# Performance work log

Measured on AMD Instinct MI355X. Metric: run time of the kernel, lower is better.

Reference implementation:

```python
import jax, jax.numpy as jnp
import numpy as np

B = 2048
PARAM_SHAPES = {
    'l1c0': (1, 8, 3, 3), 'l1c1': (3, 4, 8, 2), 'l1c2': (2, 4, 8, 2), 'l1c3': (2, 4, 8, 2), 'l1c4': (2, 4, 8, 1), 'b1': (8, 4, 4, 4, 4),
    'l2c0': (1, 4, 8, 2), 'l2c1': (2, 2, 4, 2), 'l2c2': (2, 2, 4, 2), 'l2c3': (2, 2, 4, 2), 'l2c4': (2, 2, 4, 1), 'b2': (4, 2, 2, 2, 2),
    'l3c0': (1, 2, 4, 2), 'l3c1': (2, 2, 2, 2), 'l3c2': (2, 2, 2, 2), 'l3c3': (2, 2, 2, 2), 'l3c4': (2, 2, 2, 1), 'b3': (2, 2, 2, 2, 2),
    'W': (2, 32), 'bl': (2,),
}

def setup_inputs():
    key = jax.random.key(0)
    ks = jax.random.split(key, len(PARAM_SHAPES) + 1)
    inp = {'x': jax.random.normal(ks[0], (B, 3, 8, 8, 8, 8), dtype=jnp.float32)}
    for k, (name, shp) in zip(ks[1:], PARAM_SHAPES.items()):
        scale = 0.5 if name[0] == 'l' and name != 'bl' else 0.1
        inp[name] = jax.random.normal(k, shp, dtype=jnp.float32) * scale
    return inp

def tt_linear(x, cores, bias):
    # y[b, m1..md] = sum_{n1..nd} W[m1..md, n1..nd] x[b, n1..nd] + bias[m1..md]
    # W is the TT-matrix with cores G_k of shape (r_{k-1}, m_k, n_k, r_k).
    b = x.shape[0]
    z = x.reshape(b, 1, -1)  # (B, rank, flat=[n_k..n_d, m_1..m_{k-1}])
    for G in cores:
        r0, m, n, r1 = G.shape
        z = jnp.einsum('brns,rmnq->bqsm', z.reshape(b, r0, n, -1), G).reshape(b, r1, -1)
    return z.reshape((b,) + bias.shape) + bias

def reference(x, l1c0, l1c1, l1c2, l1c3, l1c4, b1, l2c0, l2c1, l2c2, l2c3, l2c4, b2, l3c0, l3c1, l3c2, l3c3, l3c4, b3, W, bl):
    h = jax.nn.relu(tt_linear(x, [l1c0, l1c1, l1c2, l1c3, l1c4], b1))
    h = jax.nn.relu(tt_linear(h, [l2c0, l2c1, l2c2, l2c3, l2c4], b2))
    h = jax.nn.relu(tt_linear(h, [l3c0, l3c1, l3c2, l3c3, l3c4], b3))
    logits = h.reshape(-1, 32) @ W.T + bl  # (B, 2)
    return jax.nn.log_softmax(logits, axis=1)
```

## Files before the change

### kernel.cpp

```cpp
#include <hip/hip_runtime.h>
#include <math.h>

#define WC3  0
#define WC2  128
#define WU1  256
#define T2S  288
#define T3S  1440
#define H1O  288
#define BO   2528
#define CO   1440
#define DO   1984
#define H2O  2256
#define H3O  2320
#define LDS_FLOATS 3680

__global__ void tt_setup_w3(const float* __restrict__ v0, const float* __restrict__ v1,
                            const float* __restrict__ v2, const float* __restrict__ v3,
                            const float* __restrict__ v4, float* __restrict__ w3) {
    int i = blockIdx.x * 256 + threadIdx.x;
    if (i >= 2048) return;
    int mi = i >> 6, nj = i & 63;
    int m1 = (mi >> 4) & 1, m2 = (mi >> 3) & 1, m3 = (mi >> 2) & 1, m4 = (mi >> 1) & 1, m5 = mi & 1;
    int n1 = (nj >> 4) & 3, n2 = (nj >> 3) & 1, n3 = (nj >> 2) & 1, n4 = (nj >> 1) & 1, n5 = nj & 1;
    float s = 0.f;
#pragma unroll
    for (int q1 = 0; q1 < 2; ++q1) {
        float a1 = v0[(m1 * 4 + n1) * 2 + q1];
#pragma unroll
        for (int q2 = 0; q2 < 2; ++q2) {
            float a2 = a1 * v1[((q1 * 2 + m2) * 2 + n2) * 2 + q2];
#pragma unroll
            for (int q3 = 0; q3 < 2; ++q3) {
                float a3 = a2 * v2[((q2 * 2 + m3) * 2 + n3) * 2 + q3];
#pragma unroll
                for (int q4 = 0; q4 < 2; ++q4)
                    s = fmaf(a3 * v3[((q3 * 2 + m4) * 2 + n4) * 2 + q4],
                             v4[(q4 * 2 + m5) * 2 + n5], s);
            }
        }
    }
    w3[i] = s;
}

#define PREFETCH_X(BUF, SLAB) do {                                          \
    const float4* xq_ = (const float4*)xb + (SLAB) * 512 + t * 8;           \
    _Pragma("unroll")                                                       \
    for (int i_ = 0; i_ < 8; ++i_) {                                        \
        const float4 v_ = xq_[i_];                                          \
        BUF[i_*4+0] = v_.x; BUF[i_*4+1] = v_.y;                             \
        BUF[i_*4+2] = v_.z; BUF[i_*4+3] = v_.w;                             \
    } } while (0)

#define STEP1(BUF) do {                                                     \
    _Pragma("unroll") for (int m5_ = 0; m5_ < 4; ++m5_)                     \
    _Pragma("unroll") for (int q4_ = 0; q4_ < 2; ++q4_) {                   \
        const float* w_ = g4 + (q4_ * 4 + m5_) * 8;                         \
        _Pragma("unroll") for (int n4l_ = 0; n4l_ < 4; ++n4l_) {            \
            float sa_ = BUF[n4l_*8+0] * w_[0];                              \
            _Pragma("unroll") for (int n5_ = 1; n5_ < 8; ++n5_)             \
                sa_ = fmaf(BUF[n4l_*8+n5_], w_[n5_], sa_);                  \
            t1[n4l_*8 + m5_*2 + q4_] = sa_;                                 \
        } } } while (0)

__global__ __launch_bounds__(64)
__attribute__((amdgpu_waves_per_eu(1, 2)))
void tt_main(const float* __restrict__ x,
             const float* __restrict__ g0, const float* __restrict__ g1,
             const float* __restrict__ g2, const float* __restrict__ g3,
             const float* __restrict__ g4, const float* __restrict__ b1g,
             const float* __restrict__ u0, const float* __restrict__ u1,
             const float* __restrict__ u2, const float* __restrict__ u3,
             const float* __restrict__ u4, const float* __restrict__ b2g,
             const float* __restrict__ b3g,
             const float* __restrict__ Wmg, const float* __restrict__ blg,
             const float* __restrict__ w3g,
             float* __restrict__ out)
{
    __shared__ float smem[LDS_FLOATS];
    const int t = threadIdx.x;
    const int b = blockIdx.x;
    const float* xb = x + (size_t)b * 12288;

    float xv0[32], xv1[32], t1[32];

    PREFETCH_X(xv0, 0);
    PREFETCH_X(xv1, 1);

    smem[WC3 + t] = g3[t];  smem[WC3 + 64 + t] = g3[64 + t];
    smem[WC2 + t] = g2[t];  smem[WC2 + 64 + t] = g2[64 + t];
    if (t < 32) smem[WU1 + t] = u1[t];
    __syncthreads();

    const int h = t & 1;
    const int p = t >> 1;

    float regT4[36];
#pragma unroll
    for (int i = 0; i < 36; ++i) regT4[i] = 0.f;

    STEP1(xv0);

#pragma unroll
    for (int s = 0; s < 6; ++s) {
        const int n1 = s >> 1, n2h = s & 1;

        if (s < 4) {
            if (s & 1) { PREFETCH_X(xv1, s + 2); } else { PREFETCH_X(xv0, s + 2); }
        }

        float acc[16];
#pragma unroll
        for (int i = 0; i < 16; ++i) acc[i] = 0.f;
#pragma unroll
        for (int pass = 0; pass < 2; ++pass) {
            const int hh = (pass == 0) ? h : (1 - h);
            if (pass == 1) {
#pragma unroll
                for (int i = 0; i < 32; ++i) t1[i] = __shfl_xor(t1[i], 1);
            }
#pragma unroll
            for (int m4 = 0; m4 < 4; ++m4) {
                const int cbase = WC3 + ((h * 4 + m4) * 8 + hh * 4) * 2;
                const float4 c0 = *(const float4*)&smem[cbase];
                const float4 c1 = *(const float4*)&smem[cbase + 4];
                const float cs[8] = {c0.x, c0.y, c0.z, c0.w, c1.x, c1.y, c1.z, c1.w};
#pragma unroll
                for (int m5 = 0; m5 < 4; ++m5) {
                    float sa = acc[m4*4+m5];
#pragma unroll
                    for (int n4l = 0; n4l < 4; ++n4l)
#pragma unroll
                    for (int q4 = 0; q4 < 2; ++q4)
                        sa = fmaf(t1[n4l*8 + m5*2 + q4], cs[n4l*2 + q4], sa);
                    acc[m4*4+m5] = sa;
                }
            }
        }

        __syncthreads();
#pragma unroll
        for (int m45 = 0; m45 < 16; ++m45)
            smem[T2S + p * 36 + m45 * 2 + h] = acc[m45];
        __syncthreads();

        {
            const int n3h = t & 1;
            const int q2  = (t >> 1) & 1;
            const int m3  = (t >> 2) & 3;
            const int n2l = t >> 4;
            float o3[16];
#pragma unroll
            for (int i = 0; i < 16; ++i) o3[i] = 0.f;
#pragma unroll
            for (int n3l = 0; n3l < 4; ++n3l) {
                const int rb = T2S + (n2l * 8 + n3h * 4 + n3l) * 36;
                float rv[32];
#pragma unroll
                for (int g = 0; g < 8; ++g) {
                    const float4 v = *(const float4*)&smem[rb + g * 4];
                    rv[g*4+0] = v.x; rv[g*4+1] = v.y; rv[g*4+2] = v.z; rv[g*4+3] = v.w;
                }
                const int wb = WC2 + ((q2 * 4 + m3) * 8 + n3h * 4 + n3l) * 2;
                const float w0 = smem[wb], w1 = smem[wb + 1];
#pragma unroll
                for (int m45 = 0; m45 < 16; ++m45)
                    o3[m45] = fmaf(rv[m45*2], w0, fmaf(rv[m45*2+1], w1, o3[m45]));
            }
#pragma unroll
            for (int k = 0; k < 16; ++k) o3[k] += __shfl_xor(o3[k], 1);
            const int row = n2h * 16 + n2l * 4 + m3;
#pragma unroll
            for (int k = 0; k < 8; ++k) {
                const float v = n3h ? o3[8 + k] : o3[k];
                smem[T3S + row * 34 + (n3h * 8 + k) * 2 + q2] = v;
            }
        }

        if (s < 5) {
            if ((s + 1) & 1) { STEP1(xv1); } else { STEP1(xv0); }
        }

        if (n2h == 1) {
            __syncthreads();

            const int m3 = t >> 4, m4 = (t >> 2) & 3, m5 = t & 3;
            float2 zz[8];
#pragma unroll
            for (int n2 = 0; n2 < 8; ++n2)
                zz[n2] = *(const float2*)&smem[T3S + (n2 * 4 + m3) * 34 + (m4 * 4 + m5) * 2];
#pragma unroll
            for (int jj = 0; jj < 4; ++jj)
#pragma unroll
            for (int q1 = 0; q1 < 3; ++q1) {
                float sa = regT4[jj * 9 + n1 * 3 + q1];
#pragma unroll
                for (int n2g = 0; n2g < 4; ++n2g) {
                    const float4 w = *(const float4*)(g1 + ((q1 * 4 + jj) * 8 + n2g * 2) * 2);
                    sa = fmaf(zz[n2g*2].x,   w.x, sa);
                    sa = fmaf(zz[n2g*2].y,   w.y, sa);
                    sa = fmaf(zz[n2g*2+1].x, w.z, sa);
                    sa = fmaf(zz[n2g*2+1].y, w.w, sa);
                }
                regT4[jj * 9 + n1 * 3 + q1] = sa;
            }
        }
    }
    __syncthreads();

#pragma unroll
    for (int jj = 0; jj < 4; ++jj) {
        float bia[8];
#pragma unroll
        for (int m1 = 0; m1 < 8; ++m1) bia[m1] = b1g[m1 * 256 + jj * 64 + t];
#pragma unroll
        for (int m1 = 0; m1 < 8; ++m1) {
            float sa = bia[m1];
#pragma unroll
            for (int n1 = 0; n1 < 3; ++n1)
#pragma unroll
            for (int q1 = 0; q1 < 3; ++q1)
                sa = fmaf(regT4[jj * 9 + n1 * 3 + q1], g0[(m1 * 3 + n1) * 3 + q1], sa);
            smem[H1O + m1 * 256 + jj * 64 + t] = fmaxf(sa, 0.f);
        }
    }
    __syncthreads();

#pragma unroll
    for (int pq = 0; pq < 2; ++pq) {
        const int p3 = 2 * t + pq;
        float o[8];
#pragma unroll
        for (int i = 0; i < 8; ++i) o[i] = 0.f;
#pragma unroll
        for (int n4 = 0; n4 < 4; ++n4) {
            const float4 hv = *(const float4*)&smem[H1O + (p3 * 4 + n4) * 4];
            const float ax = hv.x*u4[0]  + hv.y*u4[1]  + hv.z*u4[2]  + hv.w*u4[3];
            const float ay = hv.x*u4[8]  + hv.y*u4[9]  + hv.z*u4[10] + hv.w*u4[11];
            const float az = hv.x*u4[4]  + hv.y*u4[5]  + hv.z*u4[6]  + hv.w*u4[7];
            const float aw = hv.x*u4[12] + hv.y*u4[13] + hv.z*u4[14] + hv.w*u4[15];
#pragma unroll
            for (int q4 = 0; q4 < 2; ++q4) {
                const float a0 = q4 ? ay : ax;
                const float a1 = q4 ? aw : az;
#pragma unroll
                for (int q3 = 0; q3 < 2; ++q3)
#pragma unroll
                for (int m4 = 0; m4 < 2; ++m4) {
                    const float w = u3[((q3 * 2 + m4) * 4 + n4) * 2 + q4];
                    o[(m4 * 2 + 0) * 2 + q3] = fmaf(a0, w, o[(m4 * 2 + 0) * 2 + q3]);
                    o[(m4 * 2 + 1) * 2 + q3] = fmaf(a1, w, o[(m4 * 2 + 1) * 2 + q3]);
                }
            }
        }
#pragma unroll
        for (int k = 0; k < 8; ++k) smem[BO + p3 * 9 + k] = o[k];
    }
    __syncthreads();

    if (t < 32) {
        float o[16];
#pragma unroll
        for (int i = 0; i < 16; ++i) o[i] = 0.f;
#pragma unroll
        for (int n3 = 0; n3 < 4; ++n3)
#pragma unroll
        for (int q3 = 0; q3 < 2; ++q3) {
            float zb[4];
#pragma unroll
            for (int m45 = 0; m45 < 4; ++m45)
                zb[m45] = smem[BO + (t * 4 + n3) * 9 + m45 * 2 + q3];
#pragma unroll
            for (int m3 = 0; m3 < 2; ++m3)
#pragma unroll
            for (int q2 = 0; q2 < 2; ++q2) {
                const float w = u2[((q2 * 2 + m3) * 4 + n3) * 2 + q3];
#pragma unroll
                for (int m45 = 0; m45 < 4; ++m45)
                    o[(m3 * 4 + m45) * 2 + q2] = fmaf(zb[m45], w, o[(m3 * 4 + m45) * 2 + q2]);
            }
        }
#pragma unroll
        for (int k = 0; k < 16; ++k) smem[CO + t * 17 + k] = o[k];
    }
    __syncthreads();

    if (t < 32) {
        const int n1 = t >> 2, m2 = (t >> 1) & 1, m3 = t & 1;
        float o[8];
#pragma unroll
        for (int i = 0; i < 8; ++i) o[i] = 0.f;
#pragma unroll
        for (int n2 = 0; n2 < 4; ++n2)
#pragma unroll
        for (int q2 = 0; q2 < 2; ++q2) {
            float cb[4];
#pragma unroll
            for (int m45 = 0; m45 < 4; ++m45)
                cb[m45] = smem[CO + (n1 * 4 + n2) * 17 + (m3 * 4 + m45) * 2 + q2];
#pragma unroll
            for (int q1 = 0; q1 < 2; ++q1) {
                const float w = smem[WU1 + ((q1 * 2 + m2) * 4 + n2) * 2 + q2];
#pragma unroll
                for (int m45 = 0; m45 < 4; ++m45)
                    o[m45 * 2 + q1] = fmaf(cb[m45], w, o[m45 * 2 + q1]);
            }
        }
#pragma unroll
        for (int m45 = 0; m45 < 4; ++m45)
#pragma unroll
        for (int q1 = 0; q1 < 2; ++q1)
            smem[DO + (m2 * 8 + m3 * 4 + m45) * 17 + n1 * 2 + q1] = o[m45 * 2 + q1];
    }
    __syncthreads();

    if (t < 16) {
        float o[4];
#pragma unroll
        for (int i = 0; i < 4; ++i) o[i] = 0.f;
#pragma unroll
        for (int n1 = 0; n1 < 8; ++n1)
#pragma unroll
        for (int q1 = 0; q1 < 2; ++q1) {
            const float dv = smem[DO + t * 17 + n1 * 2 + q1];
#pragma unroll
            for (int m1 = 0; m1 < 4; ++m1)
                o[m1] = fmaf(dv, u0[(m1 * 8 + n1) * 2 + q1], o[m1]);
        }
#pragma unroll
        for (int m1 = 0; m1 < 4; ++m1)
            smem[H2O + m1 * 16 + t] = fmaxf(o[m1] + b2g[m1 * 16 + t], 0.f);
    }
    __syncthreads();

    if (t < 32) {
        const float4* wr = (const float4*)(w3g + t * 64);
        float sa = b3g[t];
#pragma unroll
        for (int g = 0; g < 16; ++g) {
            const float4 w4 = wr[g];
            sa = fmaf(w4.x, smem[H2O + g*4 + 0],
                 fmaf(w4.y, smem[H2O + g*4 + 1],
                 fmaf(w4.z, smem[H2O + g*4 + 2],
                 fmaf(w4.w, smem[H2O + g*4 + 3], sa))));
        }
        smem[H3O + t] = fmaxf(sa, 0.f);
    }
    __syncthreads();

    {
        const int k = t & 31;
        float pr = smem[H3O + k] * Wmg[t];
#pragma unroll
        for (int d = 16; d >= 1; d >>= 1) pr += __shfl_xor(pr, d);
        const float l0 = __shfl(pr, 0) + blg[0];
        const float l1 = __shfl(pr, 32) + blg[1];
        if (t == 0) {
            const float mm = fmaxf(l0, l1);
            const float lse = mm + logf(expf(l0 - mm) + expf(l1 - mm));
            out[(size_t)b * 2 + 0] = l0 - lse;
            out[(size_t)b * 2 + 1] = l1 - lse;
        }
    }
}

extern "C" void kernel_launch(void* const* d_in, const int* in_sizes, int n_in,
                              void* d_out, int out_size, void* d_ws, size_t ws_size,
                              hipStream_t stream) {
    const float* x    = (const float*)d_in[0];
    const float* l1c0 = (const float*)d_in[1];
    const float* l1c1 = (const float*)d_in[2];
    const float* l1c2 = (const float*)d_in[3];
    const float* l1c3 = (const float*)d_in[4];
    const float* l1c4 = (const float*)d_in[5];
    const float* b1   = (const float*)d_in[6];
    const float* l2c0 = (const float*)d_in[7];
    const float* l2c1 = (const float*)d_in[8];
    const float* l2c2 = (const float*)d_in[9];
    const float* l2c3 = (const float*)d_in[10];
    const float* l2c4 = (const float*)d_in[11];
    const float* b2   = (const float*)d_in[12];
    const float* l3c0 = (const float*)d_in[13];
    const float* l3c1 = (const float*)d_in[14];
    const float* l3c2 = (const float*)d_in[15];
    const float* l3c3 = (const float*)d_in[16];
    const float* l3c4 = (const float*)d_in[17];
    const float* b3   = (const float*)d_in[18];
    const float* Wm   = (const float*)d_in[19];
    const float* bl   = (const float*)d_in[20];
    float* W3 = (float*)d_ws;

    tt_setup_w3<<<8, 256, 0, stream>>>(l3c0, l3c1, l3c2, l3c3, l3c4, W3);
    tt_main<<<2048, 64, 0, stream>>>(x, l1c0, l1c1, l1c2, l1c3, l1c4, b1,
                                     l2c0, l2c1, l2c2, l2c3, l2c4, b2, b3,
                                     Wm, bl, W3, (float*)d_out);
}
```

Baseline: 218.3 us.

## Process two batch samples per block to interleave independent work and halve grid

```diff
diff --git a/kernel.cpp b/kernel.cpp
--- a/kernel.cpp
+++ b/kernel.cpp
@@ -1,18 +1,26 @@
 #include <hip/hip_runtime.h>
 #include <math.h>
 
-#define WC3  0
-#define WC2  128
-#define WU1  256
-#define T2S  288
-#define T3S  1440
-#define H1O  288
-#define BO   2528
-#define CO   1440
-#define DO   1984
-#define H2O  2256
-#define H3O  2320
-#define LDS_FLOATS 3680
+#define WC3   0
+#define WC2   128
+#define WU1   256
+#define T2A_  288
+#define T3A_  1440
+#define T2B_  2528
+#define T3B_  3680
+#define H1A_  288
+#define H1B_  2528
+#define BO_A  4768
+#define BO_B  5920
+#define CO_A  7072
+#define CO_B  7616
+#define DO_A  8160
+#define DO_B  8432
+#define H2A_  8704
+#define H2B_  8768
+#define H3A_  8832
+#define H3B_  8864
+#define LDS_FLOATS 8896
 
 __global__ void tt_setup_w3(const float* __restrict__ v0, const float* __restrict__ v1,
                             const float* __restrict__ v2, const float* __restrict__ v3,
@@ -42,16 +50,15 @@
     w3[i] = s;
 }
 
-#define PREFETCH_X(BUF, SLAB) do {                                          \
-    const float4* xq_ = (const float4*)xb + (SLAB) * 512 + t * 8;           \
-    _Pragma("unroll")                                                       \
-    for (int i_ = 0; i_ < 8; ++i_) {                                        \
+#define PREFETCH_X(BUF, XB, SLAB) do {                                      \
+    const float4* xq_ = (const float4*)(XB) + (SLAB) * 512 + t * 8;         \
+    _Pragma("unroll") for (int i_ = 0; i_ < 8; ++i_) {                      \
         const float4 v_ = xq_[i_];                                          \
         BUF[i_*4+0] = v_.x; BUF[i_*4+1] = v_.y;                             \
         BUF[i_*4+2] = v_.z; BUF[i_*4+3] = v_.w;                             \
     } } while (0)
 
-#define STEP1(BUF) do {                                                     \
+#define STEP1(T1, BUF) do {                                                 \
     _Pragma("unroll") for (int m5_ = 0; m5_ < 4; ++m5_)                     \
     _Pragma("unroll") for (int q4_ = 0; q4_ < 2; ++q4_) {                   \
         const float* w_ = g4 + (q4_ * 4 + m5_) * 8;                         \
@@ -59,11 +66,97 @@
             float sa_ = BUF[n4l_*8+0] * w_[0];                              \
             _Pragma("unroll") for (int n5_ = 1; n5_ < 8; ++n5_)             \
                 sa_ = fmaf(BUF[n4l_*8+n5_], w_[n5_], sa_);                  \
-            t1[n4l_*8 + m5_*2 + q4_] = sa_;                                 \
+            T1[n4l_*8 + m5_*2 + q4_] = sa_;                                 \
         } } } while (0)
 
+#define STEP2(ACC, T1) do {                                                 \
+    _Pragma("unroll") for (int i_ = 0; i_ < 16; ++i_) ACC[i_] = 0.f;        \
+    _Pragma("unroll") for (int pass_ = 0; pass_ < 2; ++pass_) {             \
+        const int hh_ = (pass_ == 0) ? h : (1 - h);                         \
+        if (pass_ == 1) {                                                   \
+            _Pragma("unroll") for (int i_ = 0; i_ < 32; ++i_)               \
+                T1[i_] = __shfl_xor(T1[i_], 1);                             \
+        }                                                                   \
+        _Pragma("unroll") for (int m4_ = 0; m4_ < 4; ++m4_) {               \
+            const int cb_ = WC3 + ((h * 4 + m4_) * 8 + hh_ * 4) * 2;        \
+            const float4 c0_ = *(const float4*)&smem[cb_];                  \
+            const float4 c1_ = *(const float4*)&smem[cb_ + 4];              \
+            const float cs_[8] = {c0_.x,c0_.y,c0_.z,c0_.w,c1_.x,c1_.y,c1_.z,c1_.w}; \
+            _Pragma("unroll") for (int m5_ = 0; m5_ < 4; ++m5_) {           \
+                float sa_ = ACC[m4_*4+m5_];                                 \
+                _Pragma("unroll") for (int n4l_ = 0; n4l_ < 4; ++n4l_)      \
+                _Pragma("unroll") for (int q4_ = 0; q4_ < 2; ++q4_)         \
+                    sa_ = fmaf(T1[n4l_*8 + m5_*2 + q4_], cs_[n4l_*2+q4_], sa_); \
+                ACC[m4_*4+m5_] = sa_;                                       \
+            } } } } while (0)
+
+#define STEP3(T2X, T3X) do {                                                \
+    const int n3h_ = t & 1, q2_ = (t >> 1) & 1, m3_ = (t >> 2) & 3, n2l_ = t >> 4; \
+    float o3_[16];                                                          \
+    _Pragma("unroll") for (int i_ = 0; i_ < 16; ++i_) o3_[i_] = 0.f;        \
+    _Pragma("unroll") for (int n3l_ = 0; n3l_ < 4; ++n3l_) {                \
+        const int rb_ = (T2X) + (n2l_*8 + n3h_*4 + n3l_) * 36;              \
+        float rv_[32];                                                      \
+        _Pragma("unroll") for (int g_ = 0; g_ < 8; ++g_) {                  \
+            const float4 v_ = *(const float4*)&smem[rb_ + g_*4];            \
+            rv_[g_*4+0]=v_.x; rv_[g_*4+1]=v_.y; rv_[g_*4+2]=v_.z; rv_[g_*4+3]=v_.w; \
+        }                                                                   \
+        const int wb_ = WC2 + ((q2_*4 + m3_)*8 + n3h_*4 + n3l_) * 2;        \
+        const float w0_ = smem[wb_], w1_ = smem[wb_+1];                     \
+        _Pragma("unroll") for (int m45_ = 0; m45_ < 16; ++m45_)             \
+            o3_[m45_] = fmaf(rv_[m45_*2], w0_, fmaf(rv_[m45_*2+1], w1_, o3_[m45_])); \
+    }                                                                       \
+    _Pragma("unroll") for (int k_ = 0; k_ < 16; ++k_) o3_[k_] += __shfl_xor(o3_[k_], 1); \
+    const int row_ = n2h*16 + n2l_*4 + m3_;                                 \
+    _Pragma("unroll") for (int k_ = 0; k_ < 8; ++k_) {                      \
+        const float v_ = n3h_ ? o3_[8+k_] : o3_[k_];                        \
+        smem[(T3X) + row_*34 + (n3h_*8+k_)*2 + q2_] = v_;                   \
+    } } while (0)
+
+#define STEP4(T3X, RT4) do {                                                \
+    const int m3_ = t >> 4, m4_ = (t >> 2) & 3, m5_ = t & 3;                \
+    float2 zz_[8];                                                          \
+    _Pragma("unroll") for (int n2_ = 0; n2_ < 8; ++n2_)                     \
+        zz_[n2_] = *(const float2*)&smem[(T3X) + (n2_*4+m3_)*34 + (m4_*4+m5_)*2]; \
+    _Pragma("unroll") for (int jj_ = 0; jj_ < 4; ++jj_)                     \
+    _Pragma("unroll") for (int q1_ = 0; q1_ < 3; ++q1_) {                   \
+        float sa_ = RT4[jj_*9 + n1*3 + q1_];                                \
+        _Pragma("unroll") for (int n2g_ = 0; n2g_ < 4; ++n2g_) {            \
+            const float4 w_ = *(const float4*)(g1 + ((q1_*4+jj_)*8 + n2g_*2)*2); \
+            sa_ = fmaf(zz_[n2g_*2].x,   w_.x, sa_);                         \
+            sa_ = fmaf(zz_[n2g_*2].y,   w_.y, sa_);                         \
+            sa_ = fmaf(zz_[n2g_*2+1].x, w_.z, sa_);                         \
+            sa_ = fmaf(zz_[n2g_*2+1].y, w_.w, sa_);                         \
+        }                                                                   \
+        RT4[jj_*9 + n1*3 + q1_] = sa_;                                      \
+    } } while (0)
+
+#define L2AB(H1X, BOX) do {                                                 \
+    _Pragma("unroll") for (int pq_ = 0; pq_ < 2; ++pq_) {                   \
+        const int p3_ = 2*t + pq_;                                          \
+        float o_[8];                                                        \
+        _Pragma("unroll") for (int i_ = 0; i_ < 8; ++i_) o_[i_] = 0.f;      \
+        _Pragma("unroll") for (int n4_ = 0; n4_ < 4; ++n4_) {               \
+            const float4 hv_ = *(const float4*)&smem[(H1X) + (p3_*4+n4_)*4]; \
+            const float ax_ = hv_.x*u4[0]  + hv_.y*u4[1]  + hv_.z*u4[2]  + hv_.w*u4[3];  \
+            const float ay_ = hv_.x*u4[8]  + hv_.y*u4[9]  + hv_.z*u4[10] + hv_.w*u4[11]; \
+            const float az_ = hv_.x*u4[4]  + hv_.y*u4[5]  + hv_.z*u4[6]  + hv_.w*u4[7];  \
+            const float aw_ = hv_.x*u4[12] + hv_.y*u4[13] + hv_.z*u4[14] + hv_.w*u4[15]; \
+            _Pragma("unroll") for (int q4_ = 0; q4_ < 2; ++q4_) {           \
+                const float a0_ = q4_ ? ay_ : ax_;                          \
+                const float a1_ = q4_ ? aw_ : az_;                          \
+                _Pragma("unroll") for (int q3_ = 0; q3_ < 2; ++q3_)         \
+                _Pragma("unroll") for (int m4_ = 0; m4_ < 2; ++m4_) {       \
+                    const float w_ = u3[((q3_*2+m4_)*4+n4_)*2+q4_];         \
+                    o_[(m4_*2+0)*2+q3_] = fmaf(a0_, w_, o_[(m4_*2+0)*2+q3_]); \
+                    o_[(m4_*2+1)*2+q3_] = fmaf(a1_, w_, o_[(m4_*2+1)*2+q3_]); \
+                } } }                                                       \
+        _Pragma("unroll") for (int k_ = 0; k_ < 8; ++k_)                    \
+            smem[(BOX) + p3_*9 + k_] = o_[k_];                              \
+    } } while (0)
+
 __global__ __launch_bounds__(64)
-__attribute__((amdgpu_waves_per_eu(1, 2)))
+__attribute__((amdgpu_waves_per_eu(1, 1)))
 void tt_main(const float* __restrict__ x,
              const float* __restrict__ g0, const float* __restrict__ g1,
              const float* __restrict__ g2, const float* __restrict__ g3,
@@ -79,12 +172,12 @@
     __shared__ float smem[LDS_FLOATS];
     const int t = threadIdx.x;
     const int b = blockIdx.x;
-    const float* xb = x + (size_t)b * 12288;
-
-    float xv0[32], xv1[32], t1[32];
-
-    PREFETCH_X(xv0, 0);
-    PREFETCH_X(xv1, 1);
+    const float* xbA = x + (size_t)(2 * b) * 12288;
+    const float* xbB = xbA + 12288;
+
+    float xvA[32], xvB[32];
+    PREFETCH_X(xvA, xbA, 0);
+    PREFETCH_X(xvB, xbB, 0);
 
     smem[WC3 + t] = g3[t];  smem[WC3 + 64 + t] = g3[64 + t];
     smem[WC2 + t] = g2[t];  smem[WC2 + 64 + t] = g2[64 + t];
@@ -94,116 +187,42 @@
     const int h = t & 1;
     const int p = t >> 1;
 
-    float regT4[36];
-#pragma unroll
-    for (int i = 0; i < 36; ++i) regT4[i] = 0.f;
-
-    STEP1(xv0);
-
-#pragma unroll
-    for (int s = 0; s < 6; ++s) {
-        const int n1 = s >> 1, n2h = s & 1;
-
-        if (s < 4) {
-            if (s & 1) { PREFETCH_X(xv1, s + 2); } else { PREFETCH_X(xv0, s + 2); }
-        }
-
-        float acc[16];
-#pragma unroll
-        for (int i = 0; i < 16; ++i) acc[i] = 0.f;
-#pragma unroll
-        for (int pass = 0; pass < 2; ++pass) {
-            const int hh = (pass == 0) ? h : (1 - h);
-            if (pass == 1) {
-#pragma unroll
-                for (int i = 0; i < 32; ++i) t1[i] = __shfl_xor(t1[i], 1);
-            }
-#pragma unroll
-            for (int m4 = 0; m4 < 4; ++m4) {
-                const int cbase = WC3 + ((h * 4 + m4) * 8 + hh * 4) * 2;
-                const float4 c0 = *(const float4*)&smem[cbase];
-                const float4 c1 = *(const float4*)&smem[cbase + 4];
-                const float cs[8] = {c0.x, c0.y, c0.z, c0.w, c1.x, c1.y, c1.z, c1.w};
-#pragma unroll
-                for (int m5 = 0; m5 < 4; ++m5) {
-                    float sa = acc[m4*4+m5];
-#pragma unroll
-                    for (int n4l = 0; n4l < 4; ++n4l)
-#pragma unroll
-                    for (int q4 = 0; q4 < 2; ++q4)
-                        sa = fmaf(t1[n4l*8 + m5*2 + q4], cs[n4l*2 + q4], sa);
-                    acc[m4*4+m5] = sa;
-                }
-            }
-        }
-
+    float rT4A[36], rT4B[36];
+#pragma unroll
+    for (int i = 0; i < 36; ++i) { rT4A[i] = 0.f; rT4B[i] = 0.f; }
+
+#pragma unroll
+    for (int n1 = 0; n1 < 3; ++n1) {
+#pragma unroll 1
+        for (int n2h = 0; n2h < 2; ++n2h) {
+            const int s = n1 * 2 + n2h;
+
+            float t1[32];
+            float accA[16], accB[16];
+            STEP1(t1, xvA);
+            if (s < 5) PREFETCH_X(xvA, xbA, s + 1);
+            STEP2(accA, t1);
+
+            STEP1(t1, xvB);
+            if (s < 5) PREFETCH_X(xvB, xbB, s + 1);
+            STEP2(accB, t1);
+
+            __syncthreads();
+#pragma unroll
+            for (int m45 = 0; m45 < 16; ++m45)
+                smem[T2A_ + p * 36 + m45 * 2 + h] = accA[m45];
+#pragma unroll
+            for (int m45 = 0; m45 < 16; ++m45)
+                smem[T2B_ + p * 36 + m45 * 2 + h] = accB[m45];
+            __syncthreads();
+
+            STEP3(T2A_, T3A_);
+            STEP3(T2B_, T3B_);
+        }
         __syncthreads();
-#pragma unroll
-        for (int m45 = 0; m45 < 16; ++m45)
-            smem[T2S + p * 36 + m45 * 2 + h] = acc[m45];
-        __syncthreads();
-
-        {
-            const int n3h = t & 1;
-            const int q2  = (t >> 1) & 1;
-            const int m3  = (t >> 2) & 3;
-            const int n2l = t >> 4;
-            float o3[16];
-#pragma unroll
-            for (int i = 0; i < 16; ++i) o3[i] = 0.f;
-#pragma unroll
-            for (int n3l = 0; n3l < 4; ++n3l) {
-                const int rb = T2S + (n2l * 8 + n3h * 4 + n3l) * 36;
-                float rv[32];
-#pragma unroll
-                for (int g = 0; g < 8; ++g) {
-                    const float4 v = *(const float4*)&smem[rb + g * 4];
-                    rv[g*4+0] = v.x; rv[g*4+1] = v.y; rv[g*4+2] = v.z; rv[g*4+3] = v.w;
-                }
-                const int wb = WC2 + ((q2 * 4 + m3) * 8 + n3h * 4 + n3l) * 2;
-                const float w0 = smem[wb], w1 = smem[wb + 1];
-#pragma unroll
-                for (int m45 = 0; m45 < 16; ++m45)
-                    o3[m45] = fmaf(rv[m45*2], w0, fmaf(rv[m45*2+1], w1, o3[m45]));
-            }
-#pragma unroll
-            for (int k = 0; k < 16; ++k) o3[k] += __shfl_xor(o3[k], 1);
-            const int row = n2h * 16 + n2l * 4 + m3;
-#pragma unroll
-            for (int k = 0; k < 8; ++k) {
-                const float v = n3h ? o3[8 + k] : o3[k];
-                smem[T3S + row * 34 + (n3h * 8 + k) * 2 + q2] = v;
-            }
-        }
-
-        if (s < 5) {
-            if ((s + 1) & 1) { STEP1(xv1); } else { STEP1(xv0); }
-        }
-
-        if (n2h == 1) {
-            __syncthreads();
-
-            const int m3 = t >> 4, m4 = (t >> 2) & 3, m5 = t & 3;
-            float2 zz[8];
-#pragma unroll
-            for (int n2 = 0; n2 < 8; ++n2)
-                zz[n2] = *(const float2*)&smem[T3S + (n2 * 4 + m3) * 34 + (m4 * 4 + m5) * 2];
-#pragma unroll
-            for (int jj = 0; jj < 4; ++jj)
-#pragma unroll
-            for (int q1 = 0; q1 < 3; ++q1) {
-                float sa = regT4[jj * 9 + n1 * 3 + q1];
-#pragma unroll
-                for (int n2g = 0; n2g < 4; ++n2g) {
-                    const float4 w = *(const float4*)(g1 + ((q1 * 4 + jj) * 8 + n2g * 2) * 2);
-                    sa = fmaf(zz[n2g*2].x,   w.x, sa);
-                    sa = fmaf(zz[n2g*2].y,   w.y, sa);
-                    sa = fmaf(zz[n2g*2+1].x, w.z, sa);
-                    sa = fmaf(zz[n2g*2+1].y, w.w, sa);
-                }
-                regT4[jj * 9 + n1 * 3 + q1] = sa;
-            }
-        }
+
+        STEP4(T3A_, rT4A);
+        STEP4(T3B_, rT4B);
     }
     __syncthreads();
 
@@ -214,50 +233,34 @@
         for (int m1 = 0; m1 < 8; ++m1) bia[m1] = b1g[m1 * 256 + jj * 64 + t];
 #pragma unroll
         for (int m1 = 0; m1 < 8; ++m1) {
-            float sa = bia[m1];
+            float saA = bia[m1], saB = bia[m1];
 #pragma unroll
             for (int n1 = 0; n1 < 3; ++n1)
 #pragma unroll
-            for (int q1 = 0; q1 < 3; ++q1)
-                sa = fmaf(regT4[jj * 9 + n1 * 3 + q1], g0[(m1 * 3 + n1) * 3 + q1], sa);
-            smem[H1O + m1 * 256 + jj * 64 + t] = fmaxf(sa, 0.f);
-        }
-    }
-    __syncthreads();
-
-#pragma unroll
-    for (int pq = 0; pq < 2; ++pq) {
-        const int p3 = 2 * t + pq;
-        float o[8];
-#pragma unroll
-        for (int i = 0; i < 8; ++i) o[i] = 0.f;
-#pragma unroll
-        for (int n4 = 0; n4 < 4; ++n4) {
-            const float4 hv = *(const float4*)&smem[H1O + (p3 * 4 + n4) * 4];
-            const float ax = hv.x*u4[0]  + hv.y*u4[1]  + hv.z*u4[2]  + hv.w*u4[3];
-            const float ay = hv.x*u4[8]  + hv.y*u4[9]  + hv.z*u4[10] + hv.w*u4[11];
-            const float az = hv.x*u4[4]  + hv.y*u4[5]  + hv.z*u4[6]  + hv.w*u4[7];
-            const float aw = hv.x*u4[12] + hv.y*u4[13] + hv.z*u4[14] + hv.w*u4[15];
-#pragma unroll
-            for (int q4 = 0; q4 < 2; ++q4) {
-                const float a0 = q4 ? ay : ax;
-                const float a1 = q4 ? aw : az;
-#pragma unroll
-                for (int q3 = 0; q3 < 2; ++q3)
-#pragma unroll
-                for (int m4 = 0; m4 < 2; ++m4) {
-                    const float w = u3[((q3 * 2 + m4) * 4 + n4) * 2 + q4];
-                    o[(m4 * 2 + 0) * 2 + q3] = fmaf(a0, w, o[(m4 * 2 + 0) * 2 + q3]);
-                    o[(m4 * 2 + 1) * 2 + q3] = fmaf(a1, w, o[(m4 * 2 + 1) * 2 + q3]);
-                }
+            for (int q1 = 0; q1 < 3; ++q1) {
+                const float w = g0[(m1 * 3 + n1) * 3 + q1];
+                saA = fmaf(rT4A[jj * 9 + n1 * 3 + q1], w, saA);
+                saB = fmaf(rT4B[jj * 9 + n1 * 3 + q1], w, saB);
             }
-        }
-#pragma unroll
-        for (int k = 0; k < 8; ++k) smem[BO + p3 * 9 + k] = o[k];
-    }
-    __syncthreads();
-
-    if (t < 32) {
+            smem[H1A_ + m1 * 256 + jj * 64 + t] = fmaxf(saA, 0.f);
+            smem[H1B_ + m1 * 256 + jj * 64 + t] = fmaxf(saB, 0.f);
+        }
+    }
+    __syncthreads();
+
+    L2AB(H1A_, BO_A);
+    L2AB(H1B_, BO_B);
+    __syncthreads();
+
+    const int sg = t >> 5;
+    const int tt = t & 31;
+    const int BOS = sg ? BO_B : BO_A;
+    const int COS = sg ? CO_B : CO_A;
+    const int DOS = sg ? DO_B : DO_A;
+    const int H2S = sg ? H2B_ : H2A_;
+    const int H3S = sg ? H3B_ : H3A_;
+
+    {
         float o[16];
 #pragma unroll
         for (int i = 0; i < 16; ++i) o[i] = 0.f;
@@ -268,7 +271,7 @@
             float zb[4];
 #pragma unroll
             for (int m45 = 0; m45 < 4; ++m45)
-                zb[m45] = smem[BO + (t * 4 + n3) * 9 + m45 * 2 + q3];
+                zb[m45] = smem[BOS + (tt * 4 + n3) * 9 + m45 * 2 + q3];
 #pragma unroll
             for (int m3 = 0; m3 < 2; ++m3)
 #pragma unroll
@@ -280,12 +283,12 @@
             }
         }
 #pragma unroll
-        for (int k = 0; k < 16; ++k) smem[CO + t * 17 + k] = o[k];
-    }
-    __syncthreads();
-
-    if (t < 32) {
-        const int n1 = t >> 2, m2 = (t >> 1) & 1, m3 = t & 1;
+        for (int k = 0; k < 16; ++k) smem[COS + tt * 17 + k] = o[k];
+    }
+    __syncthreads();
+
+    {
+        const int n1 = tt >> 2, m2 = (tt >> 1) & 1, m3 = tt & 1;
         float o[8];
 #pragma unroll
         for (int i = 0; i < 8; ++i) o[i] = 0.f;
@@ -296,7 +299,7 @@
             float cb[4];
 #pragma unroll
             for (int m45 = 0; m45 < 4; ++m45)
-                cb[m45] = smem[CO + (n1 * 4 + n2) * 17 + (m3 * 4 + m45) * 2 + q2];
+                cb[m45] = smem[COS + (n1 * 4 + n2) * 17 + (m3 * 4 + m45) * 2 + q2];
 #pragma unroll
             for (int q1 = 0; q1 < 2; ++q1) {
                 const float w = smem[WU1 + ((q1 * 2 + m2) * 4 + n2) * 2 + q2];
@@ -309,11 +312,11 @@
         for (int m45 = 0; m45 < 4; ++m45)
 #pragma unroll
         for (int q1 = 0; q1 < 2; ++q1)
-            smem[DO + (m2 * 8 + m3 * 4 + m45) * 17 + n1 * 2 + q1] = o[m45 * 2 + q1];
-    }
-    __syncthreads();
-
-    if (t < 16) {
+            smem[DOS + (m2 * 8 + m3 * 4 + m45) * 17 + n1 * 2 + q1] = o[m45 * 2 + q1];
+    }
+    __syncthreads();
+
+    if (tt < 16) {
         float o[4];
 #pragma unroll
         for (int i = 0; i < 4; ++i) o[i] = 0.f;
@@ -321,44 +324,49 @@
         for (int n1 = 0; n1 < 8; ++n1)
 #pragma unroll
         for (int q1 = 0; q1 < 2; ++q1) {
-            const float dv = smem[DO + t * 17 + n1 * 2 + q1];
+            const float dv = smem[DOS + tt * 17 + n1 * 2 + q1];
 #pragma unroll
             for (int m1 = 0; m1 < 4; ++m1)
                 o[m1] = fmaf(dv, u0[(m1 * 8 + n1) * 2 + q1], o[m1]);
         }
 #pragma unroll
         for (int m1 = 0; m1 < 4; ++m1)
-            smem[H2O + m1 * 16 + t] = fmaxf(o[m1] + b2g[m1 * 16 + t], 0.f);
-    }
-    __syncthreads();
-
-    if (t < 32) {
-        const float4* wr = (const float4*)(w3g + t * 64);
-        float sa = b3g[t];
-#pragma unroll
-        for (int g = 0; g < 16; ++g) {
-            const float4 w4 = wr[g];
-            sa = fmaf(w4.x, smem[H2O + g*4 + 0],
-                 fmaf(w4.y, smem[H2O + g*4 + 1],
-                 fmaf(w4.z, smem[H2O + g*4 + 2],
-                 fmaf(w4.w, smem[H2O + g*4 + 3], sa))));
-        }
-        smem[H3O + t] = fmaxf(sa, 0.f);
+            smem[H2S + m1 * 16 + tt] = fmaxf(o[m1] + b2g[m1 * 16 + tt], 0.f);
     }
     __syncthreads();
 
     {
-        const int k = t & 31;
-        float pr = smem[H3O + k] * Wmg[t];
-#pragma unroll
-        for (int d = 16; d >= 1; d >>= 1) pr += __shfl_xor(pr, d);
-        const float l0 = __shfl(pr, 0) + blg[0];
-        const float l1 = __shfl(pr, 32) + blg[1];
-        if (t == 0) {
+        const float4* wr = (const float4*)(w3g + tt * 64);
+        float sa = b3g[tt];
+#pragma unroll
+        for (int gg = 0; gg < 16; ++gg) {
+            const float4 w4 = wr[gg];
+            sa = fmaf(w4.x, smem[H2S + gg*4 + 0],
+                 fmaf(w4.y, smem[H2S + gg*4 + 1],
+                 fmaf(w4.z, smem[H2S + gg*4 + 2],
+                 fmaf(w4.w, smem[H2S + gg*4 + 3], sa))));
+        }
+        smem[H3S + tt] = fmaxf(sa, 0.f);
+    }
+    __syncthreads();
+
+    {
+        const float h3v = smem[H3S + tt];
+        float pr0 = h3v * Wmg[tt];
+        float pr1 = h3v * Wmg[32 + tt];
+#pragma unroll
+        for (int d = 16; d >= 1; d >>= 1) {
+            pr0 += __shfl_xor(pr0, d);
+            pr1 += __shfl_xor(pr1, d);
+        }
+        if (tt == 0) {
+            const float l0 = pr0 + blg[0];
+            const float l1 = pr1 + blg[1];
             const float mm = fmaxf(l0, l1);
             const float lse = mm + logf(expf(l0 - mm) + expf(l1 - mm));
-            out[(size_t)b * 2 + 0] = l0 - lse;
-            out[(size_t)b * 2 + 1] = l1 - lse;
+            const size_t bb = (size_t)(2 * b + sg);
+            out[bb * 2 + 0] = l0 - lse;
+            out[bb * 2 + 1] = l1 - lse;
         }
     }
 }
@@ -390,7 +398,7 @@
     float* W3 = (float*)d_ws;
 
     tt_setup_w3<<<8, 256, 0, stream>>>(l3c0, l3c1, l3c2, l3c3, l3c4, W3);
-    tt_main<<<2048, 64, 0, stream>>>(x, l1c0, l1c1, l1c2, l1c3, l1c4, b1,
+    tt_main<<<1024, 64, 0, stream>>>(x, l1c0, l1c1, l1c2, l1c3, l1c4, b1,
                                      l2c0, l2c1, l2c2, l2c3, l2c4, b2, b3,
                                      Wm, bl, W3, (float*)d_out);
 }
```

After: 218.0 us. About the same (-0.1%).

## Process two slabs per iteration with double T2 buffers to halve barriers

Applied to the files above, without the earlier changes.

```diff
diff --git a/kernel.cpp b/kernel.cpp
--- a/kernel.cpp
+++ b/kernel.cpp
@@ -4,15 +4,16 @@
 #define WC3  0
 #define WC2  128
 #define WU1  256
-#define T2S  288
-#define T3S  1440
+#define T2A_ 288
+#define T2B_ 1440
+#define T3S  2592
 #define H1O  288
-#define BO   2528
-#define CO   1440
-#define DO   1984
-#define H2O  2256
-#define H3O  2320
-#define LDS_FLOATS 3680
+#define BO   2592
+#define CO   288
+#define DO   832
+#define H2O  1104
+#define H3O  1168
+#define LDS_FLOATS 3744
 
 __global__ void tt_setup_w3(const float* __restrict__ v0, const float* __restrict__ v1,
                             const float* __restrict__ v2, const float* __restrict__ v3,
@@ -44,14 +45,13 @@
 
 #define PREFETCH_X(BUF, SLAB) do {                                          \
     const float4* xq_ = (const float4*)xb + (SLAB) * 512 + t * 8;           \
-    _Pragma("unroll")                                                       \
-    for (int i_ = 0; i_ < 8; ++i_) {                                        \
+    _Pragma("unroll") for (int i_ = 0; i_ < 8; ++i_) {                      \
         const float4 v_ = xq_[i_];                                          \
         BUF[i_*4+0] = v_.x; BUF[i_*4+1] = v_.y;                             \
         BUF[i_*4+2] = v_.z; BUF[i_*4+3] = v_.w;                             \
     } } while (0)
 
-#define STEP1(BUF) do {                                                     \
+#define STEP1(T1, BUF) do {                                                 \
     _Pragma("unroll") for (int m5_ = 0; m5_ < 4; ++m5_)                     \
     _Pragma("unroll") for (int q4_ = 0; q4_ < 2; ++q4_) {                   \
         const float* w_ = g4 + (q4_ * 4 + m5_) * 8;                         \
@@ -59,8 +59,52 @@
             float sa_ = BUF[n4l_*8+0] * w_[0];                              \
             _Pragma("unroll") for (int n5_ = 1; n5_ < 8; ++n5_)             \
                 sa_ = fmaf(BUF[n4l_*8+n5_], w_[n5_], sa_);                  \
-            t1[n4l_*8 + m5_*2 + q4_] = sa_;                                 \
+            T1[n4l_*8 + m5_*2 + q4_] = sa_;                                 \
         } } } while (0)
+
+#define STEP2(ACC, T1) do {                                                 \
+    _Pragma("unroll") for (int i_ = 0; i_ < 16; ++i_) ACC[i_] = 0.f;        \
+    _Pragma("unroll") for (int pass_ = 0; pass_ < 2; ++pass_) {             \
+        const int hh_ = (pass_ == 0) ? h : (1 - h);                         \
+        if (pass_ == 1) {                                                   \
+            _Pragma("unroll") for (int i_ = 0; i_ < 32; ++i_)               \
+                T1[i_] = __shfl_xor(T1[i_], 1);                             \
+        }                                                                   \
+        _Pragma("unroll") for (int m4_ = 0; m4_ < 4; ++m4_) {               \
+            const int cb_ = WC3 + ((h * 4 + m4_) * 8 + hh_ * 4) * 2;        \
+            const float4 c0_ = *(const float4*)&smem[cb_];                  \
+            const float4 c1_ = *(const float4*)&smem[cb_ + 4];              \
+            const float cs_[8] = {c0_.x,c0_.y,c0_.z,c0_.w,c1_.x,c1_.y,c1_.z,c1_.w}; \
+            _Pragma("unroll") for (int m5_ = 0; m5_ < 4; ++m5_) {           \
+                float sa_ = ACC[m4_*4+m5_];                                 \
+                _Pragma("unroll") for (int n4l_ = 0; n4l_ < 4; ++n4l_)      \
+                _Pragma("unroll") for (int q4_ = 0; q4_ < 2; ++q4_)         \
+                    sa_ = fmaf(T1[n4l_*8 + m5_*2 + q4_], cs_[n4l_*2+q4_], sa_); \
+                ACC[m4_*4+m5_] = sa_;                                       \
+            } } } } while (0)
+
+#define STEP3(T2X, ROWBASE) do {                                            \
+    const int n3h_ = t & 1, q2_ = (t >> 1) & 1, m3_ = (t >> 2) & 3, n2l_ = t >> 4; \
+    float o3_[16];                                                          \
+    _Pragma("unroll") for (int i_ = 0; i_ < 16; ++i_) o3_[i_] = 0.f;        \
+    _Pragma("unroll") for (int n3l_ = 0; n3l_ < 4; ++n3l_) {                \
+        const int rb_ = (T2X) + (n2l_*8 + n3h_*4 + n3l_) * 36;              \
+        float rv_[32];                                                      \
+        _Pragma("unroll") for (int g_ = 0; g_ < 8; ++g_) {                  \
+            const float4 v_ = *(const float4*)&smem[rb_ + g_*4];            \
+            rv_[g_*4+0]=v_.x; rv_[g_*4+1]=v_.y; rv_[g_*4+2]=v_.z; rv_[g_*4+3]=v_.w; \
+        }                                                                   \
+        const int wb_ = WC2 + ((q2_*4 + m3_)*8 + n3h_*4 + n3l_) * 2;        \
+        const float w0_ = smem[wb_], w1_ = smem[wb_+1];                     \
+        _Pragma("unroll") for (int m45_ = 0; m45_ < 16; ++m45_)             \
+            o3_[m45_] = fmaf(rv_[m45_*2], w0_, fmaf(rv_[m45_*2+1], w1_, o3_[m45_])); \
+    }                                                                       \
+    _Pragma("unroll") for (int k_ = 0; k_ < 16; ++k_) o3_[k_] += __shfl_xor(o3_[k_], 1); \
+    const int row_ = (ROWBASE) + n2l_*4 + m3_;                              \
+    _Pragma("unroll") for (int k_ = 0; k_ < 8; ++k_) {                      \
+        const float v_ = n3h_ ? o3_[8+k_] : o3_[k_];                        \
+        smem[T3S + row_*34 + (n3h_*8+k_)*2 + q2_] = v_;                     \
+    } } while (0)
 
 __global__ __launch_bounds__(64)
 __attribute__((amdgpu_waves_per_eu(1, 2)))
@@ -81,8 +125,7 @@
     const int b = blockIdx.x;
     const float* xb = x + (size_t)b * 12288;
 
-    float xv0[32], xv1[32], t1[32];
-
+    float xv0[32], xv1[32];
     PREFETCH_X(xv0, 0);
     PREFETCH_X(xv1, 1);
 
@@ -98,91 +141,30 @@
 #pragma unroll
     for (int i = 0; i < 36; ++i) regT4[i] = 0.f;
 
-    STEP1(xv0);
-
-#pragma unroll
-    for (int s = 0; s < 6; ++s) {
-        const int n1 = s >> 1, n2h = s & 1;
-
-        if (s < 4) {
-            if (s & 1) { PREFETCH_X(xv1, s + 2); } else { PREFETCH_X(xv0, s + 2); }
-        }
-
-        float acc[16];
-#pragma unroll
-        for (int i = 0; i < 16; ++i) acc[i] = 0.f;
-#pragma unroll
-        for (int pass = 0; pass < 2; ++pass) {
-            const int hh = (pass == 0) ? h : (1 - h);
-            if (pass == 1) {
-#pragma unroll
-                for (int i = 0; i < 32; ++i) t1[i] = __shfl_xor(t1[i], 1);
-            }
-#pragma unroll
-            for (int m4 = 0; m4 < 4; ++m4) {
-                const int cbase = WC3 + ((h * 4 + m4) * 8 + hh * 4) * 2;
-                const float4 c0 = *(const float4*)&smem[cbase];
-                const float4 c1 = *(const float4*)&smem[cbase + 4];
-                const float cs[8] = {c0.x, c0.y, c0.z, c0.w, c1.x, c1.y, c1.z, c1.w};
-#pragma unroll
-                for (int m5 = 0; m5 < 4; ++m5) {
-                    float sa = acc[m4*4+m5];
-#pragma unroll
-                    for (int n4l = 0; n4l < 4; ++n4l)
-#pragma unroll
-                    for (int q4 = 0; q4 < 2; ++q4)
-                        sa = fmaf(t1[n4l*8 + m5*2 + q4], cs[n4l*2 + q4], sa);
-                    acc[m4*4+m5] = sa;
-                }
-            }
-        }
+#pragma unroll
+    for (int n1 = 0; n1 < 3; ++n1) {
+        float t1[32], accA[16], accB[16];
+        STEP1(t1, xv0);
+        if (n1 < 2) PREFETCH_X(xv0, 2 * n1 + 2);
+        STEP2(accA, t1);
+        STEP1(t1, xv1);
+        if (n1 < 2) PREFETCH_X(xv1, 2 * n1 + 3);
+        STEP2(accB, t1);
 
         __syncthreads();
 #pragma unroll
         for (int m45 = 0; m45 < 16; ++m45)
-            smem[T2S + p * 36 + m45 * 2 + h] = acc[m45];
+            smem[T2A_ + p * 36 + m45 * 2 + h] = accA[m45];
+#pragma unroll
+        for (int m45 = 0; m45 < 16; ++m45)
+            smem[T2B_ + p * 36 + m45 * 2 + h] = accB[m45];
         __syncthreads();
 
+        STEP3(T2A_, 0);
+        STEP3(T2B_, 16);
+        __syncthreads();
+
         {
-            const int n3h = t & 1;
-            const int q2  = (t >> 1) & 1;
-            const int m3  = (t >> 2) & 3;
-            const int n2l = t >> 4;
-            float o3[16];
-#pragma unroll
-            for (int i = 0; i < 16; ++i) o3[i] = 0.f;
-#pragma unroll
-            for (int n3l = 0; n3l < 4; ++n3l) {
-                const int rb = T2S + (n2l * 8 + n3h * 4 + n3l) * 36;
-                float rv[32];
-#pragma unroll
-                for (int g = 0; g < 8; ++g) {
-                    const float4 v = *(const float4*)&smem[rb + g * 4];
-                    rv[g*4+0] = v.x; rv[g*4+1] = v.y; rv[g*4+2] = v.z; rv[g*4+3] = v.w;
-                }
-                const int wb = WC2 + ((q2 * 4 + m3) * 8 + n3h * 4 + n3l) * 2;
-                const float w0 = smem[wb], w1 = smem[wb + 1];
-#pragma unroll
-                for (int m45 = 0; m45 < 16; ++m45)
-                    o3[m45] = fmaf(rv[m45*2], w0, fmaf(rv[m45*2+1], w1, o3[m45]));
-            }
-#pragma unroll
-            for (int k = 0; k < 16; ++k) o3[k] += __shfl_xor(o3[k], 1);
-            const int row = n2h * 16 + n2l * 4 + m3;
-#pragma unroll
-            for (int k = 0; k < 8; ++k) {
-                const float v = n3h ? o3[8 + k] : o3[k];
-                smem[T3S + row * 34 + (n3h * 8 + k) * 2 + q2] = v;
-            }
-        }
-
-        if (s < 5) {
-            if ((s + 1) & 1) { STEP1(xv1); } else { STEP1(xv0); }
-        }
-
-        if (n2h == 1) {
-            __syncthreads();
-
             const int m3 = t >> 4, m4 = (t >> 2) & 3, m5 = t & 3;
             float2 zz[8];
 #pragma unroll
```

Result: no change. 218.4 us (+0.1%).
